# Optimization experiments

Hardware: AMD Instinct MI355X
Metric: run time of the kernel (lower is better)

Reference implementation:

```python
import jax, jax.numpy as jnp
import numpy as np

# pywt db4 decomposition filters (dec_lo, dec_hi), 8 taps
DEC_LO = np.array([-0.010597401784997278, 0.032883011666982945, 0.030841381835986965,
                   -0.18703481171888114, -0.02798376941698385, 0.6308807679295904,
                   0.7148465705525415, 0.23037781330885523])
DEC_HI = np.array([-0.23037781330885523, 0.7148465705525415, -0.6308807679295904,
                   -0.02798376941698385, 0.18703481171888114, 0.030841381835986965,
                   -0.032883011666982945, -0.010597401784997278])
HEADS = 8


def dwt_db4(v):
    # Equivalent of pywt.dwt(v, 'db4') (mode='symmetric') applied along last axis.
    # Symmetric (half-point) extension by L-1=7, full convolution, downsample taking
    # every 2nd sample starting at conv index 1 -> out_len = floor((n+7)/2).
    pad = [(0, 0)] * (v.ndim - 1) + [(7, 7)]
    ext = jnp.pad(v, pad, mode='symmetric')[..., 1:]
    lead = v.shape[:-1]
    lhs = ext.reshape(-1, 1, ext.shape[-1])                       # (N, 1, n+13)
    rhs = jnp.stack([jnp.asarray(DEC_LO[::-1], v.dtype),
                     jnp.asarray(DEC_HI[::-1], v.dtype)])[:, None, :]  # (2, 1, 8)
    out = jax.lax.conv_general_dilated(lhs, rhs, (2,), 'VALID')   # (N, 2, out_len)
    out = out.reshape(*lead, 2, -1)
    return out[..., 0, :], out[..., 1, :]


def setup_inputs() -> dict:
    key = jax.random.key(0)
    k0, k1, k2, k3 = jax.random.split(key, 4)
    B, S, H = 4, 2048, 1024
    a = float(np.sqrt(6.0 / (H + H)))  # xavier_uniform bound
    x = jax.random.normal(k0, (B, S, H), dtype=jnp.float32)
    Wq = jax.random.uniform(k1, (H, H), jnp.float32, -a, a)
    Wk = jax.random.uniform(k2, (H, H), jnp.float32, -a, a)
    Wv = jax.random.uniform(k3, (H, H), jnp.float32, -a, a)
    return {"x": x, "Wq": Wq, "Wk": Wk, "Wv": Wv}


def reference(x, Wq, Wk, Wv):
    B, S, Hd = x.shape
    H = HEADS
    dk = Hd // H
    scale = dk ** -0.5
    # torch nn.Linear: y = x @ W.T
    q = (x @ Wq.T).reshape(B, S, H, dk).transpose(0, 2, 1, 3) * scale  # (B,H,S,dk)
    k = (x @ Wk.T).reshape(B, S, H, dk).transpose(0, 2, 1, 3)
    v = (x @ Wv.T).reshape(B, S, H, dk).transpose(0, 2, 1, 3)
    attn = jax.nn.softmax(jnp.einsum('bhqd,bhkd->bhqk', q, k), axis=-1)
    cA, cD = dwt_db4(v)                                   # (B,H,S,wA) each
    wA = cA.shape[-1]
    wcD = jnp.einsum('bhqk,bhkw->bhqw', attn, cD)
    out1 = wcD.transpose(0, 2, 1, 3).reshape(B, S, H * wA)
    out2 = cA.reshape(-1, S, H * wA)                      # faithful raw view of (B,H,S,wA)
    return out1, out2
```

## Files before the change

kernel.cpp:

```cpp
#include <hip/hip_runtime.h>
#include <hip/hip_bf16.h>

#define B_ 4
#define S_ 2048
#define HD 1024
#define NH 8
#define DK 128
#define WA 67
#define WPAD 80

typedef __attribute__((ext_vector_type(8))) short short8;
typedef __attribute__((ext_vector_type(4))) short short4v;
typedef __attribute__((ext_vector_type(4))) float floatx4;

__device__ __forceinline__ float hexp2(float x) { return __builtin_amdgcn_exp2f(x); }

__device__ __forceinline__ short f2bf(float f) {
    union { float f; unsigned u; } c; c.f = f;
    unsigned u = c.u;
    u += 0x7FFF + ((u >> 16) & 1);
    return (short)(u >> 16);
}
__device__ __forceinline__ float bf2f(short s) {
    union { unsigned u; float f; } c; c.u = ((unsigned)(unsigned short)s) << 16;
    return c.f;
}
__device__ __forceinline__ short f2bf_trunc(float f) {
    union { float f; unsigned u; } c; c.f = f;
    return (short)(c.u >> 16);
}

__device__ __forceinline__ void glds16(void* lds, const void* g) {
    __builtin_amdgcn_global_load_lds(
        (const __attribute__((address_space(1))) unsigned*)g,
        (__attribute__((address_space(3))) unsigned*)lds, 16, 0, 0);
}

__device__ __constant__ float FLO[8] = {
    0.23037781330885523f,  0.7148465705525415f,  0.6308807679295904f,
   -0.02798376941698385f, -0.18703481171888114f, 0.030841381835986965f,
    0.032883011666982945f, -0.010597401784997278f };
__device__ __constant__ float FHI[8] = {
   -0.010597401784997278f, -0.032883011666982945f, 0.030841381835986965f,
    0.18703481171888114f,  -0.02798376941698385f, -0.6308807679295904f,
    0.7148465705525415f,   -0.23037781330885523f };

__global__ __launch_bounds__(256) void cvt_all(
    const float* __restrict__ x,  const float* __restrict__ wq,
    const float* __restrict__ wk, const float* __restrict__ wv,
    short* __restrict__ xb, short* __restrict__ wb)
{
    const size_t w_elems = (size_t)HD * HD;
    int blk = blockIdx.x;
    const float* src; short* dst; int lb;
    if (blk < 4096)      { src = x;  dst = xb;               lb = blk; }
    else if (blk < 4608) { src = wq; dst = wb;               lb = blk - 4096; }
    else if (blk < 5120) { src = wk; dst = wb + w_elems;     lb = blk - 4608; }
    else                 { src = wv; dst = wb + 2 * w_elems; lb = blk - 5120; }
    int i = lb * 256 + threadIdx.x;
    const float4* s = (const float4*)src + (size_t)i * 2;
    float4 f0 = s[0], f1 = s[1];
    short8 o;
    o[0] = f2bf(f0.x); o[1] = f2bf(f0.y); o[2] = f2bf(f0.z); o[3] = f2bf(f0.w);
    o[4] = f2bf(f1.x); o[5] = f2bf(f1.y); o[6] = f2bf(f1.z); o[7] = f2bf(f1.w);
    *((short8*)dst + i) = o;
}

__global__ __launch_bounds__(256) void qkv_gemm(
    const short* __restrict__ xb, const short* __restrict__ Wb,
    short* __restrict__ Qb, short* __restrict__ Kb, short* __restrict__ Vb)
{
    __shared__ __align__(16) short As[128 * 64];
    __shared__ __align__(16) short Bs[128 * 64];
    const int tid  = threadIdx.x;
    const int wv   = tid >> 6;
    const int lane = tid & 63;
    const int l15  = lane & 15;
    const int quad = lane >> 4;
    const int m0 = blockIdx.x * 128;
    const int n0 = blockIdx.y * 128;
    const int z  = blockIdx.z;
    const short* W = Wb + (size_t)z * HD * HD;
    short* Yb      = (z == 0) ? Qb : (z == 1) ? Kb : Vb;
    const float scale = (z == 0) ? 0.12751743786072596f : 1.0f;
    const int wm = (wv & 1) * 64;
    const int wn = (wv >> 1) * 64;
    const int srow = lane >> 3;
    const int sch  = (lane & 7) ^ (srow & 7);
    const int rxor = (l15 & 7);

    floatx4 acc[4][4] = {};
    for (int kk = 0; kk < HD; kk += 64) {
        __syncthreads();
        #pragma unroll
        for (int i = 0; i < 4; ++i) {
            int ti = wv * 4 + i;
            int r  = ti * 8 + srow;
            glds16(As + ti * 512, xb + (size_t)(m0 + r) * HD + kk + sch * 8);
            glds16(Bs + ti * 512, W  + (size_t)(n0 + r) * HD + kk + sch * 8);
        }
        __syncthreads();
        #pragma unroll
        for (int s4 = 0; s4 < 2; ++s4) {
            short8 a[4], b[4];
            #pragma unroll
            for (int t = 0; t < 4; ++t) {
                int ch = (s4 * 4 + quad) ^ rxor;
                a[t] = *(const short8*)&As[(wm + t * 16 + l15) * 64 + ch * 8];
                b[t] = *(const short8*)&Bs[(wn + t * 16 + l15) * 64 + ch * 8];
            }
            #pragma unroll
            for (int mt = 0; mt < 4; ++mt)
                #pragma unroll
                for (int nt = 0; nt < 4; ++nt)
                    acc[mt][nt] = __builtin_amdgcn_mfma_f32_16x16x32_bf16(
                        a[mt], b[nt], acc[mt][nt], 0, 0, 0);
        }
    }
    #pragma unroll
    for (int mt = 0; mt < 4; ++mt)
        #pragma unroll
        for (int nt = 0; nt < 4; ++nt)
            #pragma unroll
            for (int reg = 0; reg < 4; ++reg) {
                int rg = m0 + wm + mt * 16 + quad * 4 + reg;
                int cg = n0 + wn + nt * 16 + l15;
                int b = rg >> 11, s = rg & 2047;
                int h = cg >> 7,  d = cg & 127;
                Yb[((size_t)(b * NH + h) * S_ + s) * DK + d] = f2bf(acc[mt][nt][reg] * scale);
            }
}

__global__ __launch_bounds__(256) void dwt_kernel(
    const short* __restrict__ Vb, float* __restrict__ outA, short* __restrict__ cdt)
{
    __shared__ float cAs[64][69];
    const int tid   = threadIdx.x;
    const int rl    = tid & 63;
    const int chunk = tid >> 6;
    const int gid = blockIdx.x * 64 + rl;
    const int bh  = gid >> 11;
    const int s   = gid & 2047;
    const short* vr = Vb + (size_t)gid * DK;
    auto getv = [&](int i) -> float {
        int k = (i < 6) ? (5 - i) : (i < 134) ? (i - 6) : (261 - i);
        return bf2f(vr[k]);
    };
    const int t0 = chunk * 17;
    const int t1 = (chunk == 3) ? WA : (t0 + 17);
    float win[8];
    #pragma unroll
    for (int j = 0; j < 8; ++j) win[j] = getv(2 * t0 + j);
    for (int t = t0; t < t1; ++t) {
        float lo = 0.f, hi = 0.f;
        #pragma unroll
        for (int j = 0; j < 8; ++j) { lo += win[j] * FLO[j]; hi += win[j] * FHI[j]; }
        cAs[rl][t] = lo;
        cdt[((size_t)bh * WPAD + t) * S_ + s] = f2bf(hi);
        #pragma unroll
        for (int j = 0; j < 6; ++j) win[j] = win[j + 2];
        if (t + 1 < t1) { win[6] = getv(2 * t + 8); win[7] = getv(2 * t + 9); }
    }
    if (chunk == 3) {
        #pragma unroll
        for (int w = WA; w < WPAD; ++w)
            cdt[((size_t)bh * WPAD + w) * S_ + s] = 0;
    }
    __syncthreads();
    float* dst = outA + (size_t)blockIdx.x * (64 * WA);
    for (int i = tid; i < (64 * WA) / 4; i += 256) {
        int f = i * 4;
        float4 v;
        v.x = cAs[(f + 0) / WA][(f + 0) % WA];
        v.y = cAs[(f + 1) / WA][(f + 1) % WA];
        v.z = cAs[(f + 2) / WA][(f + 2) % WA];
        v.w = cAs[(f + 3) / WA][(f + 3) % WA];
        *(float4*)&dst[f] = v;
    }
}

__global__ __launch_bounds__(256, 2) void attn_kernel(
    const short* __restrict__ Qb, const short* __restrict__ Kb,
    const short* __restrict__ cdt, float* __restrict__ out1)
{
    __shared__ __align__(16) short Ks[2][64 * 128];
    __shared__ __align__(16) short Ds[2][WPAD * 64];
    __shared__ __align__(16) short Pt[8 * 1024];
    const int tid  = threadIdx.x;
    const int wv   = tid >> 6;
    const int lane = tid & 63;
    const int l15  = lane & 15;
    const int quad = lane >> 4;
    const int qt = blockIdx.x;
    const int bh = blockIdx.y;
    const int b = bh >> 3, h = bh & 7;
    const int rxor = l15 & 7;

    short8 aq[2][4];
    #pragma unroll
    for (int n = 0; n < 2; ++n) {
        const short* qrow =
            Qb + ((size_t)bh * S_ + qt * 128 + wv * 32 + n * 16 + l15) * DK;
        #pragma unroll
        for (int s4 = 0; s4 < 4; ++s4)
            aq[n][s4] = *(const short8*)(qrow + s4 * 32 + quad * 8);
    }

    floatx4 O[2][5] = {};
    float lst[2] = {};

    const short* kbase = Kb + (size_t)bh * S_ * DK;
    const int krow = lane >> 4;
    const int kch  = (lane & 15);
    const int drow = lane >> 3;
    const int dch  = (lane & 7) ^ (drow & 7);
    short* ptw = Pt + wv * 2048;

    auto stage = [&](int buf, int kt) {
        #pragma unroll
        for (int i = 0; i < 4; ++i) {
            int ti = wv * 4 + i;
            int r  = ti * 4 + krow;
            int ch = kch ^ (r & 7);
            glds16(Ks[buf] + ti * 512, kbase + ((size_t)kt * 64 + r) * DK + ch * 8);
        }
        #pragma unroll
        for (int i = 0; i < 3; ++i) {
            int t = wv + i * 4;
            if (t < 10) {
                int r = t * 8 + drow;
                glds16(Ds[buf] + t * 512,
                       cdt + ((size_t)bh * WPAD + r) * S_ + kt * 64 + dch * 8);
            }
        }
    };

    stage(0, 0);
    __syncthreads();

    for (int kt = 0; kt < 32; ++kt) {
        const int cur = kt & 1;
        if (kt + 1 < 32) stage(cur ^ 1, kt + 1);

        floatx4 sc[2][4] = {};
        #pragma unroll
        for (int s4 = 0; s4 < 4; ++s4) {
            short8 kf[4];
            #pragma unroll
            for (int mt = 0; mt < 4; ++mt) {
                int ch = (s4 * 4 + quad) ^ rxor;
                kf[mt] = *(const short8*)&Ks[cur][(mt * 16 + l15) * 128 + ch * 8];
            }
            #pragma unroll
            for (int n = 0; n < 2; ++n)
                #pragma unroll
                for (int mt = 0; mt < 4; ++mt)
                    sc[n][mt] = __builtin_amdgcn_mfma_f32_16x16x32_bf16(
                        kf[mt], aq[n][s4], sc[n][mt], 0, 0, 0);
        }
        #pragma unroll
        for (int n = 0; n < 2; ++n) {
            #pragma unroll
            for (int mt = 0; mt < 4; ++mt) {
                short4v pk;
                #pragma unroll
                for (int reg = 0; reg < 4; ++reg) {
                    float p = hexp2(sc[n][mt][reg]);
                    lst[n] += p;
                    pk[reg] = f2bf_trunc(p);
                }
                int ch = (mt * 2 + (quad >> 1)) ^ rxor;
                *(short4v*)&ptw[n * 1024 + l15 * 64 + ch * 8 + (quad & 1) * 4] = pk;
            }
        }
        short8 ap[2][2];
        #pragma unroll
        for (int mt = 0; mt < 2; ++mt)
            #pragma unroll
            for (int ks = 0; ks < 2; ++ks) {
                int ch = (ks * 4 + quad) ^ rxor;
                ap[mt][ks] = *(const short8*)&ptw[mt * 1024 + l15 * 64 + ch * 8];
            }
        #pragma unroll
        for (int j = 0; j < 5; ++j) {
            #pragma unroll
            for (int ks = 0; ks < 2; ++ks) {
                int ch = (ks * 4 + quad) ^ rxor;
                short8 bd = *(const short8*)&Ds[cur][(j * 16 + l15) * 64 + ch * 8];
                #pragma unroll
                for (int mt = 0; mt < 2; ++mt)
                    O[mt][j] = __builtin_amdgcn_mfma_f32_16x16x32_bf16(
                        ap[mt][ks], bd, O[mt][j], 0, 0, 0);
            }
        }
        __syncthreads();
    }
    #pragma unroll
    for (int n = 0; n < 2; ++n) {
        float l = lst[n];
        l += __shfl_xor(l, 16, 64);
        l += __shfl_xor(l, 32, 64);
        lst[n] = l;
    }
    float rl[2][4];
    #pragma unroll
    for (int mt = 0; mt < 2; ++mt)
        #pragma unroll
        for (int reg = 0; reg < 4; ++reg)
            rl[mt][reg] = 1.0f / __shfl(lst[mt], quad * 4 + reg, 16);
    #pragma unroll
    for (int mt = 0; mt < 2; ++mt)
        #pragma unroll
        for (int j = 0; j < 5; ++j) {
            int w = j * 16 + l15;
            if (w < WA) {
                #pragma unroll
                for (int reg = 0; reg < 4; ++reg) {
                    int qrow_g = qt * 128 + wv * 32 + mt * 16 + quad * 4 + reg;
                    out1[((size_t)(b * S_ + qrow_g)) * (NH * WA) + h * WA + w] =
                        O[mt][j][reg] * rl[mt][reg];
                }
            }
        }
}

extern "C" void kernel_launch(void* const* d_in, const int* in_sizes, int n_in,
                              void* d_out, int out_size, void* d_ws, size_t ws_size,
                              hipStream_t stream)
{
    const float* x  = (const float*)d_in[0];
    const float* Wq = (const float*)d_in[1];
    const float* Wk = (const float*)d_in[2];
    const float* Wv = (const float*)d_in[3];
    float* out = (float*)d_out;

    const size_t x_elems   = (size_t)B_ * S_ * HD;
    const size_t w_elems   = (size_t)HD * HD;
    const size_t qkv_elems = (size_t)B_ * NH * S_ * DK;
    short* xb  = (short*)d_ws;
    short* Wb  = xb + x_elems;
    short* Qb  = Wb + 3 * w_elems;
    short* Kb  = Qb + qkv_elems;
    short* Vb  = Kb + qkv_elems;
    short* cdt = Vb + qkv_elems;
    float* out1 = out;
    float* out2 = out + (size_t)B_ * S_ * NH * WA;

    cvt_all<<<dim3(5632), 256, 0, stream>>>(x, Wq, Wk, Wv, xb, Wb);
    qkv_gemm<<<dim3(64, 8, 3), 256, 0, stream>>>(xb, Wb, Qb, Kb, Vb);
    dwt_kernel<<<dim3(1024), 256, 0, stream>>>(Vb, out2, cdt);
    attn_kernel<<<dim3(16, 32), 256, 0, stream>>>(Qb, Kb, cdt, out1);
}
```

Baseline: 237.4 us.

## Split attention over key halves with ones-column denominator and combine kernel

The attention kernel now splits the key range in two (split-K), doubling the grid to 1024 blocks. Each block writes bf16 partial numerators plus a row-sum column, and a new combine kernel adds the halves and divides. The softmax denominator is computed by MFMA against a column of ones that the DWT kernel writes into the padded cD buffer (WPAD raised to 96). Double buffering of the K and cD tiles is removed and the occupancy hint is raised from 2 to 3 blocks. This trades an extra kernel launch, a partial-result round trip through the workspace, bf16 rounding of the partials, and exposed load latency for more parallelism.

```diff
diff --git a/kernel.cpp b/kernel.cpp
--- a/kernel.cpp
+++ b/kernel.cpp
@@ -7,7 +7,7 @@
 #define NH 8
 #define DK 128
 #define WA 67
-#define WPAD 80
+#define WPAD 96
 
 typedef __attribute__((ext_vector_type(8))) short short8;
 typedef __attribute__((ext_vector_type(4))) short short4v;
@@ -164,7 +164,8 @@
     if (chunk == 3) {
         #pragma unroll
         for (int w = WA; w < WPAD; ++w)
-            cdt[((size_t)bh * WPAD + w) * S_ + s] = 0;
+            cdt[((size_t)bh * WPAD + w) * S_ + s] =
+                (w == 80) ? (short)0x3F80 : (short)0;
     }
     __syncthreads();
     float* dst = outA + (size_t)blockIdx.x * (64 * WA);
@@ -179,21 +180,21 @@
     }
 }
 
-__global__ __launch_bounds__(256, 2) void attn_kernel(
+__global__ __launch_bounds__(256, 3) void attn_kernel(
     const short* __restrict__ Qb, const short* __restrict__ Kb,
-    const short* __restrict__ cdt, float* __restrict__ out1)
-{
-    __shared__ __align__(16) short Ks[2][64 * 128];
-    __shared__ __align__(16) short Ds[2][WPAD * 64];
+    const short* __restrict__ cdt, short* __restrict__ pbuf)
+{
+    __shared__ __align__(16) short Ks[64 * 128];
+    __shared__ __align__(16) short Ds[WPAD * 64];
     __shared__ __align__(16) short Pt[8 * 1024];
     const int tid  = threadIdx.x;
     const int wv   = tid >> 6;
     const int lane = tid & 63;
     const int l15  = lane & 15;
     const int quad = lane >> 4;
-    const int qt = blockIdx.x;
+    const int qt   = blockIdx.x >> 1;
+    const int half = blockIdx.x & 1;
     const int bh = blockIdx.y;
-    const int b = bh >> 3, h = bh & 7;
     const int rxor = l15 & 7;
 
     short8 aq[2][4];
@@ -206,8 +207,7 @@
             aq[n][s4] = *(const short8*)(qrow + s4 * 32 + quad * 8);
     }
 
-    floatx4 O[2][5] = {};
-    float lst[2] = {};
+    floatx4 O[2][6] = {};
 
     const short* kbase = Kb + (size_t)bh * S_ * DK;
     const int krow = lane >> 4;
@@ -216,31 +216,23 @@
     const int dch  = (lane & 7) ^ (drow & 7);
     short* ptw = Pt + wv * 2048;
 
-    auto stage = [&](int buf, int kt) {
+    for (int kt = half * 16; kt < half * 16 + 16; ++kt) {
+        __syncthreads();
         #pragma unroll
         for (int i = 0; i < 4; ++i) {
             int ti = wv * 4 + i;
             int r  = ti * 4 + krow;
             int ch = kch ^ (r & 7);
-            glds16(Ks[buf] + ti * 512, kbase + ((size_t)kt * 64 + r) * DK + ch * 8);
+            glds16(Ks + ti * 512, kbase + ((size_t)kt * 64 + r) * DK + ch * 8);
         }
         #pragma unroll
         for (int i = 0; i < 3; ++i) {
             int t = wv + i * 4;
-            if (t < 10) {
-                int r = t * 8 + drow;
-                glds16(Ds[buf] + t * 512,
-                       cdt + ((size_t)bh * WPAD + r) * S_ + kt * 64 + dch * 8);
-            }
-        }
-    };
-
-    stage(0, 0);
-    __syncthreads();
-
-    for (int kt = 0; kt < 32; ++kt) {
-        const int cur = kt & 1;
-        if (kt + 1 < 32) stage(cur ^ 1, kt + 1);
+            int r = t * 8 + drow;
+            glds16(Ds + t * 512,
+                   cdt + ((size_t)bh * WPAD + r) * S_ + kt * 64 + dch * 8);
+        }
+        __syncthreads();
 
         floatx4 sc[2][4] = {};
         #pragma unroll
@@ -249,7 +241,7 @@
             #pragma unroll
             for (int mt = 0; mt < 4; ++mt) {
                 int ch = (s4 * 4 + quad) ^ rxor;
-                kf[mt] = *(const short8*)&Ks[cur][(mt * 16 + l15) * 128 + ch * 8];
+                kf[mt] = *(const short8*)&Ks[(mt * 16 + l15) * 128 + ch * 8];
             }
             #pragma unroll
             for (int n = 0; n < 2; ++n)
@@ -264,11 +256,8 @@
             for (int mt = 0; mt < 4; ++mt) {
                 short4v pk;
                 #pragma unroll
-                for (int reg = 0; reg < 4; ++reg) {
-                    float p = hexp2(sc[n][mt][reg]);
-                    lst[n] += p;
-                    pk[reg] = f2bf_trunc(p);
-                }
+                for (int reg = 0; reg < 4; ++reg)
+                    pk[reg] = f2bf_trunc(hexp2(sc[n][mt][reg]));
                 int ch = (mt * 2 + (quad >> 1)) ^ rxor;
                 *(short4v*)&ptw[n * 1024 + l15 * 64 + ch * 8 + (quad & 1) * 4] = pk;
             }
@@ -282,46 +271,48 @@
                 ap[mt][ks] = *(const short8*)&ptw[mt * 1024 + l15 * 64 + ch * 8];
             }
         #pragma unroll
-        for (int j = 0; j < 5; ++j) {
+        for (int j = 0; j < 6; ++j) {
             #pragma unroll
             for (int ks = 0; ks < 2; ++ks) {
                 int ch = (ks * 4 + quad) ^ rxor;
-                short8 bd = *(const short8*)&Ds[cur][(j * 16 + l15) * 64 + ch * 8];
+                short8 bd = *(const short8*)&Ds[(j * 16 + l15) * 64 + ch * 8];
                 #pragma unroll
                 for (int mt = 0; mt < 2; ++mt)
                     O[mt][j] = __builtin_amdgcn_mfma_f32_16x16x32_bf16(
                         ap[mt][ks], bd, O[mt][j], 0, 0, 0);
             }
         }
-        __syncthreads();
-    }
-    #pragma unroll
-    for (int n = 0; n < 2; ++n) {
-        float l = lst[n];
-        l += __shfl_xor(l, 16, 64);
-        l += __shfl_xor(l, 32, 64);
-        lst[n] = l;
-    }
-    float rl[2][4];
+    }
+    short* pb = pbuf + ((size_t)(half * 32 + bh) * S_) * 68;
     #pragma unroll
     for (int mt = 0; mt < 2; ++mt)
         #pragma unroll
-        for (int reg = 0; reg < 4; ++reg)
-            rl[mt][reg] = 1.0f / __shfl(lst[mt], quad * 4 + reg, 16);
-    #pragma unroll
-    for (int mt = 0; mt < 2; ++mt)
-        #pragma unroll
-        for (int j = 0; j < 5; ++j) {
+        for (int j = 0; j < 6; ++j) {
             int w = j * 16 + l15;
-            if (w < WA) {
-                #pragma unroll
-                for (int reg = 0; reg < 4; ++reg) {
-                    int qrow_g = qt * 128 + wv * 32 + mt * 16 + quad * 4 + reg;
-                    out1[((size_t)(b * S_ + qrow_g)) * (NH * WA) + h * WA + w] =
-                        O[mt][j][reg] * rl[mt][reg];
-                }
-            }
-        }
+            #pragma unroll
+            for (int reg = 0; reg < 4; ++reg) {
+                int qrow = qt * 128 + wv * 32 + mt * 16 + quad * 4 + reg;
+                if (w < WA)
+                    pb[(size_t)qrow * 68 + w] = f2bf(O[mt][j][reg]);
+                else if (w == 80)
+                    pb[(size_t)qrow * 68 + 67] = f2bf(O[mt][j][reg]);
+            }
+        }
+}
+
+__global__ __launch_bounds__(256) void combine_kernel(
+    const short* __restrict__ pbuf, float* __restrict__ out1)
+{
+    unsigned idx = blockIdx.x * 256 + threadIdx.x;
+    unsigned bhq = idx / 67;
+    unsigned w   = idx - bhq * 67;
+    unsigned bh  = bhq >> 11, q = bhq & 2047;
+    const short* a = pbuf + (size_t)bh * S_ * 68 + (size_t)q * 68;
+    const short* c = a + (size_t)32 * S_ * 68;
+    float num = bf2f(a[w]) + bf2f(c[w]);
+    float den = bf2f(a[67]) + bf2f(c[67]);
+    unsigned b = bh >> 3, h = bh & 7;
+    out1[((size_t)(b * S_ + q)) * (NH * WA) + h * WA + w] = num / den;
 }
 
 extern "C" void kernel_launch(void* const* d_in, const int* in_sizes, int n_in,
@@ -343,11 +334,13 @@
     short* Kb  = Qb + qkv_elems;
     short* Vb  = Kb + qkv_elems;
     short* cdt = Vb + qkv_elems;
+    short* pbuf = xb;
     float* out1 = out;
     float* out2 = out + (size_t)B_ * S_ * NH * WA;
 
     cvt_all<<<dim3(5632), 256, 0, stream>>>(x, Wq, Wk, Wv, xb, Wb);
     qkv_gemm<<<dim3(64, 8, 3), 256, 0, stream>>>(xb, Wb, Qb, Kb, Vb);
     dwt_kernel<<<dim3(1024), 256, 0, stream>>>(Vb, out2, cdt);
-    attn_kernel<<<dim3(16, 32), 256, 0, stream>>>(Qb, Kb, cdt, out1);
-}
+    attn_kernel<<<dim3(32, 32), 256, 0, stream>>>(Qb, Kb, cdt, pbuf);
+    combine_kernel<<<dim3(17152), 256, 0, stream>>>(pbuf, out1);
+}
```

New measurement: 249.6 us. 1.05x slower.
